# Optimization experiments

Measured on AMD Instinct MI355X. Metric: run time of the kernel, lower is better.

Reference implementation:

```python
import jax, jax.numpy as jnp
import numpy as np

NUM_HEADS = 8
HEAD_DIM = 64
AVG_K_LENGTH = 20
SCALE = 1.0 / (HEAD_DIM ** 0.5 * float(np.log(AVG_K_LENGTH)))  # 1/(sqrt(dim)*log(avg_k_length))


def setup_inputs() -> dict:
    key = jax.random.key(0)
    k1, k2, k3, k4 = jax.random.split(key, 4)
    B, HD, LQ, LK = 4, NUM_HEADS * HEAD_DIM, 2048, 2048
    q = jax.random.normal(k1, (B, HD, LQ), dtype=jnp.float32)
    k = jax.random.normal(k2, (B, HD, LK), dtype=jnp.float32)
    v = jax.random.normal(k3, (B, HD, LK), dtype=jnp.float32)
    k_length = jax.random.randint(k4, (B,), 512, LK + 1, dtype=jnp.int32)
    return {"q": q, "k": k, "v": v, "k_length": k_length}


def reference(q, k, v, k_length):
    b, hd, lq = q.shape
    lk = k.shape[-1]
    d = hd // NUM_HEADS
    # b (h d) l -> b h d l
    qh = q.reshape(b, NUM_HEADS, d, lq)
    kh = k.reshape(b, NUM_HEADS, d, lk)
    vh = v.reshape(b, NUM_HEADS, d, lk)
    # per-batch entropy-invariance scale: scale * log(k_length)
    s = SCALE * jnp.log(k_length.astype(jnp.float32))[:, None, None, None]  # (b,1,1,1)
    attn = jnp.einsum('bhdq,bhdk->bhqk', qh, kh)  # (b,h,lq,lk)
    attn = jax.nn.softmax(s * attn, axis=-1)
    out = jnp.einsum('bhqk,bhdk->bhdq', attn, vh)  # (b,h,d,lq)
    return out.reshape(b, hd, lq)
```

## Files before the change

kernel.cpp:

```cpp
#include <hip/hip_runtime.h>
#include <hip/hip_bf16.h>
#include <math.h>


typedef __attribute__((ext_vector_type(8))) short short8_t;
typedef __attribute__((ext_vector_type(4))) short short4_t;
typedef __attribute__((ext_vector_type(4))) float float4_t;
typedef __attribute__((ext_vector_type(16))) float float16_t;

#define SEQ   2048
#define NBH   32
#define NKT   32

__device__ __forceinline__ unsigned f2bf2u(float a, float b) {
#if __has_builtin(__builtin_amdgcn_cvt_pk_bf16_f32)
  typedef __bf16 bf16x2_t __attribute__((ext_vector_type(2)));
  union { bf16x2_t v; unsigned u; } cv;
  cv.v = __builtin_amdgcn_cvt_pk_bf16_f32(a, b);
  return cv.u;
#else
  union { float f; unsigned u; } x, y;
  x.f = a; y.f = b;
  unsigned ra = x.u + 0x7fffu + ((x.u >> 16) & 1u);
  unsigned rb = y.u + 0x7fffu + ((y.u >> 16) & 1u);
  return (ra >> 16) | (rb & 0xffff0000u);
#endif
}

__device__ __forceinline__ short f2bf1(float a) {
  return (short)(f2bf2u(a, a) & 0xffffu);
}

__device__ __forceinline__ float fast_exp2(float x) {
#if __has_builtin(__builtin_amdgcn_exp2f)
  return __builtin_amdgcn_exp2f(x);
#else
  return exp2f(x);
#endif
}

__device__ __forceinline__ void gld16(const void* g, void* l) {
  __builtin_amdgcn_global_load_lds(
      (const __attribute__((address_space(1))) void*)g,
      (__attribute__((address_space(3))) void*)l, 16, 0, 0);
}

__device__ __forceinline__ float4_t mfma32(short8_t a, short8_t b, float4_t c) {
  return __builtin_amdgcn_mfma_f32_16x16x32_bf16(a, b, c, 0, 0, 0);
}

__device__ __forceinline__ float16_t mfma3232(short8_t a, short8_t b, float16_t c) {
  return __builtin_amdgcn_mfma_f32_32x32x16_bf16(a, b, c, 0, 0, 0);
}

__device__ __forceinline__ void plswap(unsigned& a, unsigned& b, int hi) {
#if __has_builtin(__builtin_amdgcn_permlane32_swap)
  typedef __attribute__((ext_vector_type(2))) unsigned uint2_t;
  uint2_t r = __builtin_amdgcn_permlane32_swap(a, b, false, false);
  a = r[0]; b = r[1];
#else
  const unsigned sa = (unsigned)__shfl_xor((int)a, 32);
  const unsigned sb = (unsigned)__shfl_xor((int)b, 32);
  const unsigned an = hi ? sb : a;
  const unsigned bn = hi ? b : sa;
  a = an; b = bn;
#endif
}

#define PST 68
__global__ __launch_bounds__(256, 8)
void eia_prep_kernel(const float* __restrict__ kg, const float* __restrict__ vg,
                     unsigned short* __restrict__ Kt2, unsigned short* __restrict__ Vt2) {
  __shared__ __align__(16) short T[64 * PST];
  const int bh = blockIdx.x >> 5;
  const int kt = blockIdx.x & 31;
  const int t  = threadIdx.x;

  {
    const int dr = t >> 4;
    const int kq = (t & 15) * 4;
#pragma unroll
    for (int i = 0; i < 4; ++i) {
      const int d = i * 16 + dr;
      const float4_t f = *(const float4_t*)
          &kg[((size_t)bh * 64 + d) * SEQ + (size_t)(kt * 64 + kq)];
      T[(kq + 0) * PST + d] = f2bf1(f[0]);
      T[(kq + 1) * PST + d] = f2bf1(f[1]);
      T[(kq + 2) * PST + d] = f2bf1(f[2]);
      T[(kq + 3) * PST + d] = f2bf1(f[3]);
    }
  }
  __syncthreads();
  {
    unsigned short* outt = Kt2 + (size_t)(bh * 32 + kt) * 4096;
#pragma unroll
    for (int rep = 0; rep < 2; ++rep) {
      const int id2 = rep * 256 + t;
      const int lr = id2 & 63, ch = id2 >> 6;
      union { short8_t v; short4_t h[2]; } o;
      o.h[0] = *(const short4_t*)&T[lr * PST + ch * 8];
      o.h[1] = *(const short4_t*)&T[lr * PST + ch * 8 + 4];
      *(short8_t*)&outt[ch * 512 + lr * 8] = o.v;
    }
  }
  __syncthreads();

#pragma unroll
  for (int rep = 0; rep < 4; ++rep) {
    const int id2 = rep * 256 + t;
    const int d = id2 >> 4, l4 = (id2 & 15) * 4;
    const float4_t f = *(const float4_t*)
        &vg[((size_t)bh * 64 + d) * SEQ + (size_t)(kt * 64 + l4)];
    union { short4_t s; unsigned u[2]; } p;
    p.u[0] = f2bf2u(f[0], f[1]);
    p.u[1] = f2bf2u(f[2], f[3]);
    *(short4_t*)&T[d * PST + l4] = p.s;
  }
  __syncthreads();
  {
    unsigned short* outt = Vt2 + (size_t)(bh * 32 + kt) * 4096;
#pragma unroll
    for (int rep = 0; rep < 2; ++rep) {
      const int c = rep * 256 + t;
      const int kc = c >> 6, d = c & 63;
      union { short8_t v; short4_t h[2]; } o;
      o.h[0] = *(const short4_t*)&T[d * PST + kc * 8];
      o.h[1] = *(const short4_t*)&T[d * PST + kc * 8 + 4];
      *(short8_t*)&outt[c * 8] = o.v;
    }
  }
}

__global__ __launch_bounds__(256, 2)
void eia_attn_kernel(const float* __restrict__ qg,
                     const unsigned short* __restrict__ Kt2,
                     const unsigned short* __restrict__ Vt2,
                     const int* __restrict__ klen,
                     float* __restrict__ outg) {
  __shared__ __align__(16) short SM[24576];

  const int tid   = threadIdx.x;
  const int bh    = blockIdx.x & 31;
  const int qt    = blockIdx.x >> 5;
  const int q0    = qt * 128;
  const int qw    = tid >> 6;
  const int lane  = tid & 63;
  const int l31   = lane & 31;
  const int hi    = lane >> 5;

  const float c = (1.4426950408889634f / (8.0f * 2.9957322735539909f)) *
                  logf((float)klen[bh >> 3]);
  const size_t qb = (size_t)bh * 64 * SEQ;

#pragma unroll
  for (int rep = 0; rep < 8; ++rep) {
    const int id = rep * 256 + tid;
    const int d  = id >> 5;
    const int q4 = (id & 31) * 4;
    const float4_t f = *(const float4_t*)&qg[qb + (size_t)d * SEQ + (size_t)(q0 + q4)];
    SM[(q4 + 0) * 68 + d] = f2bf1(c * f[0]);
    SM[(q4 + 1) * 68 + d] = f2bf1(c * f[1]);
    SM[(q4 + 2) * 68 + d] = f2bf1(c * f[2]);
    SM[(q4 + 3) * 68 + d] = f2bf1(c * f[3]);
  }
  __syncthreads();

  short8_t qfrag[4];
#pragma unroll
  for (int s = 0; s < 4; ++s) {
    const short* qp = &SM[(qw * 32 + l31) * 68 + s * 16 + hi * 8];
    const short4_t lo = *(const short4_t*)qp;
    const short4_t hh = *(const short4_t*)(qp + 4);
    qfrag[s] = short8_t{lo[0], lo[1], lo[2], lo[3], hh[0], hh[1], hh[2], hh[3]};
  }
  __syncthreads();

  const char* ksrc = (const char*)Kt2 + (size_t)bh * NKT * 8192 + (2 * qw) * 1024 + lane * 16;
  const char* vsrc = (const char*)Vt2 + (size_t)bh * NKT * 8192 + (2 * qw) * 1024 + lane * 16;
  short* const kdst = &SM[(2 * qw) * 512];
  short* const vdst = &SM[12288 + (2 * qw) * 512];

  const int lofs = hi * 512 + l31 * 8;

  const float16_t z16 = {0.f,0.f,0.f,0.f,0.f,0.f,0.f,0.f,
                         0.f,0.f,0.f,0.f,0.f,0.f,0.f,0.f};
  float16_t oacc0 = z16, oacc1 = z16;
  float ls = 0.f;

  gld16(ksrc, kdst);               gld16(ksrc + 1024, kdst + 512);
  gld16(vsrc, vdst);               gld16(vsrc + 1024, vdst + 512);
  gld16(ksrc + 8192, kdst + 4096); gld16(ksrc + 8192 + 1024, kdst + 4096 + 512);
  gld16(vsrc + 8192, vdst + 4096); gld16(vsrc + 8192 + 1024, vdst + 4096 + 512);
  asm volatile("s_waitcnt vmcnt(0)" ::: "memory");

  int  sc = 0;
  int  sn = 2;
  size_t gsrc = 2 * 8192;

  for (int kt = 0; kt < NKT; ++kt) {
    if (kt < NKT - 1) asm volatile("s_waitcnt vmcnt(4)" ::: "memory");
    else              asm volatile("s_waitcnt vmcnt(0)" ::: "memory");
    asm volatile("s_barrier" ::: "memory");

    if (kt < NKT - 2) {
      const int so = sn * 4096;
      gld16(ksrc + gsrc, kdst + so); gld16(ksrc + gsrc + 1024, kdst + so + 512);
      gld16(vsrc + gsrc, vdst + so); gld16(vsrc + gsrc + 1024, vdst + so + 512);
      gsrc += 8192;
      sn = (sn == 2) ? 0 : sn + 1;
    }
    const int koff = sc * 4096;
    sc = (sc == 2) ? 0 : sc + 1;
    const short* const kb_ = &SM[koff + lofs];
    const short* const vb_ = &SM[12288 + koff + lofs];

    float16_t s0 = z16, s1 = z16;
#pragma unroll
    for (int s = 0; s < 4; ++s)
      s0 = mfma3232(*(const short8_t*)(kb_ + s * 1024), qfrag[s], s0);
#pragma unroll
    for (int s = 0; s < 4; ++s)
      s1 = mfma3232(*(const short8_t*)(kb_ + 256 + s * 1024), qfrag[s], s1);

    union pfu { short8_t s8; unsigned u[4]; };
    pfu pf[4];
#pragma unroll
    for (int kb = 0; kb < 2; ++kb) {
      float e[16];
#pragma unroll
      for (int r = 0; r < 16; ++r)
        e[r] = fast_exp2(kb == 0 ? s0[r] : s1[r]);
      ls += (((e[0] + e[1]) + (e[2] + e[3])) + ((e[4] + e[5]) + (e[6] + e[7]))) +
            (((e[8] + e[9]) + (e[10] + e[11])) + ((e[12] + e[13]) + (e[14] + e[15])));
#pragma unroll
      for (int ksl = 0; ksl < 2; ++ksl) {
        const int b = ksl * 8;
        unsigned a02 = f2bf2u(e[b + 0], e[b + 1]);
        unsigned b02 = f2bf2u(e[b + 4], e[b + 5]);
        unsigned a13 = f2bf2u(e[b + 2], e[b + 3]);
        unsigned b13 = f2bf2u(e[b + 6], e[b + 7]);
        plswap(a02, b02, hi);
        plswap(a13, b13, hi);
        pf[kb * 2 + ksl].u[0] = a02;
        pf[kb * 2 + ksl].u[1] = a13;
        pf[kb * 2 + ksl].u[2] = b02;
        pf[kb * 2 + ksl].u[3] = b13;
      }
    }

#pragma unroll
    for (int ks = 0; ks < 4; ++ks)
      oacc0 = mfma3232(*(const short8_t*)(vb_ + ks * 1024), pf[ks].s8, oacc0);
#pragma unroll
    for (int ks = 0; ks < 4; ++ks)
      oacc1 = mfma3232(*(const short8_t*)(vb_ + 256 + ks * 1024), pf[ks].s8, oacc1);
  }

  const float lst = ls + __shfl_xor(ls, 32);
  const float inv = 1.0f / lst;
  const size_t ob = qb + (size_t)(q0 + qw * 32 + l31);
#pragma unroll
  for (int r = 0; r < 16; ++r) {
    const int drow = (r & 3) + 8 * (r >> 2) + 4 * hi;
    outg[ob + (size_t)(drow) * SEQ]      = oacc0[r] * inv;
    outg[ob + (size_t)(drow + 32) * SEQ] = oacc1[r] * inv;
  }
}

#define DPAD  72
#define PPAD  68
__global__ __launch_bounds__(256, 5)
void eia_attn_fb(const float* __restrict__ qg, const float* __restrict__ kg,
                 const float* __restrict__ vg, const int* __restrict__ klen,
                 float* __restrict__ outg) {
  __shared__ __align__(16) short QPs[64 * DPAD];
  __shared__ __align__(16) short Ksf[64 * DPAD];
  __shared__ __align__(16) short Vsf[64 * DPAD];

  const int tid  = threadIdx.x;
  const int bh   = blockIdx.x & 31;
  const int qt   = blockIdx.x >> 5;
  const int q0   = qt * 64;
  const int w    = tid >> 6;
  const int lane = tid & 63;
  const int quad = lane >> 4;
  const int l16  = lane & 15;

  const size_t base = (size_t)bh * 64 * SEQ;
  const float c = (1.4426950408889634f / (8.0f * 2.9957322735539909f)) *
                  logf((float)klen[bh >> 3]);

#pragma unroll
  for (int it = 0; it < 2; ++it) {
    const int e = it * 4 + w;
    float f[8];
#pragma unroll
    for (int j = 0; j < 8; ++j)
      f[j] = c * qg[base + (size_t)(e * 8 + j) * SEQ + (size_t)(q0 + lane)];
    union { short8_t s8; unsigned u[4]; } t;
#pragma unroll
    for (int j = 0; j < 4; ++j) t.u[j] = f2bf2u(f[2 * j], f[2 * j + 1]);
    *(short8_t*)&QPs[lane * DPAD + e * 8] = t.s8;
  }
  __syncthreads();

  short8_t qfrag[2];
#pragma unroll
  for (int s = 0; s < 2; ++s)
    qfrag[s] = *(const short8_t*)&QPs[(w * 16 + l16) * DPAD + s * 32 + quad * 8];

  float4_t oacc[4];
#pragma unroll
  for (int t = 0; t < 4; ++t) { oacc[t][0] = 0.f; oacc[t][1] = 0.f; oacc[t][2] = 0.f; oacc[t][3] = 0.f; }
  float lsumv[4] = {0.f, 0.f, 0.f, 0.f};
  const int pbase = w * (16 * DPAD);

  for (int kt = 0; kt < NKT; ++kt) {
    const int k0 = kt * 64;
#pragma unroll
    for (int it = 0; it < 2; ++it) {
      float f[8];
#pragma unroll
      for (int j = 0; j < 8; ++j)
        f[j] = kg[base + (size_t)((it * 4 + w) * 8 + j) * SEQ + (size_t)(k0 + lane)];
      union { short8_t s8; unsigned u[4]; } t;
#pragma unroll
      for (int j = 0; j < 4; ++j) t.u[j] = f2bf2u(f[2 * j], f[2 * j + 1]);
      *(short8_t*)&Ksf[lane * DPAD + (it * 4 + w) * 8] = t.s8;
    }
#pragma unroll
    for (int it = 0; it < 4; ++it) {
      const int d = it * 16 + (w << 2) + (lane >> 4);
      const float4_t vv = *(const float4_t*)&vg[base + (size_t)d * SEQ + (size_t)(k0 + ((lane & 15) << 2))];
      union { short4_t s4; unsigned u[2]; } t;
      t.u[0] = f2bf2u(vv[0], vv[1]);
      t.u[1] = f2bf2u(vv[2], vv[3]);
      *(short4_t*)&Vsf[d * DPAD + ((lane & 15) << 2)] = t.s4;
    }
    __syncthreads();

    float4_t sacc[4];
#pragma unroll
    for (int t = 0; t < 4; ++t) { sacc[t][0] = 0.f; sacc[t][1] = 0.f; sacc[t][2] = 0.f; sacc[t][3] = 0.f; }
#pragma unroll
    for (int t = 0; t < 4; ++t)
#pragma unroll
      for (int s = 0; s < 2; ++s) {
        const short8_t bf = *(const short8_t*)&Ksf[(t * 16 + l16) * DPAD + s * 32 + quad * 8];
        sacc[t] = mfma32(qfrag[s], bf, sacc[t]);
      }

#pragma unroll
    for (int r = 0; r < 4; ++r) {
      const float p0 = fast_exp2(sacc[0][r]);
      const float p1 = fast_exp2(sacc[1][r]);
      const float p2 = fast_exp2(sacc[2][r]);
      const float p3 = fast_exp2(sacc[3][r]);
      lsumv[r] += (p0 + p1) + (p2 + p3);
      const int prow = pbase + (quad * 4 + r) * PPAD + l16;
      QPs[prow +  0] = f2bf1(p0);
      QPs[prow + 16] = f2bf1(p1);
      QPs[prow + 32] = f2bf1(p2);
      QPs[prow + 48] = f2bf1(p3);
    }

#pragma unroll
    for (int s = 0; s < 2; ++s) {
      const short* pr = &QPs[pbase + l16 * PPAD + s * 32 + quad * 8];
      const short4_t plo = *(const short4_t*)pr;
      const short4_t phi = *(const short4_t*)(pr + 4);
      const short8_t pfv = {plo[0], plo[1], plo[2], plo[3], phi[0], phi[1], phi[2], phi[3]};
#pragma unroll
      for (int t = 0; t < 4; ++t) {
        const short8_t vf = *(const short8_t*)&Vsf[(t * 16 + l16) * DPAD + s * 32 + quad * 8];
        oacc[t] = mfma32(pfv, vf, oacc[t]);
      }
    }
    __syncthreads();
  }

  float inv[4];
#pragma unroll
  for (int r = 0; r < 4; ++r) {
    float v = lsumv[r];
    v += __shfl_xor(v, 1);
    v += __shfl_xor(v, 2);
    v += __shfl_xor(v, 4);
    v += __shfl_xor(v, 8);
    inv[r] = 1.0f / v;
  }
#pragma unroll
  for (int t = 0; t < 4; ++t)
#pragma unroll
    for (int r = 0; r < 4; ++r)
      outg[base + (size_t)(t * 16 + l16) * SEQ +
           (size_t)(q0 + w * 16 + quad * 4 + r)] = oacc[t][r] * inv[r];
}

extern "C" void kernel_launch(void* const* d_in, const int* in_sizes, int n_in,
                              void* d_out, int out_size, void* d_ws, size_t ws_size,
                              hipStream_t stream) {
  const float* q  = (const float*)d_in[0];
  const float* k  = (const float*)d_in[1];
  const float* v  = (const float*)d_in[2];
  const int*   kl = (const int*)d_in[3];
  float* out = (float*)d_out;

  const size_t TEN  = (size_t)NBH * SEQ * 64;
  const size_t need = 2 * TEN * sizeof(unsigned short);

  if (ws_size >= need) {
    unsigned short* Kt2 = (unsigned short*)d_ws;
    unsigned short* Vt2 = Kt2 + TEN;
    eia_prep_kernel<<<1024, 256, 0, stream>>>(k, v, Kt2, Vt2);
    eia_attn_kernel<<<512, 256, 0, stream>>>(q, Kt2, Vt2, kl, out);
  } else {
    eia_attn_fb<<<1024, 256, 0, stream>>>(q, k, v, kl, out);
  }
}
```

Baseline: 139.6 us.

## Halve attention block size and load V directly into registers with double buffering

Each block now has 2 waves covering 64 queries, down from 4 waves covering 128, and twice as many blocks are launched. V tiles no longer pass through LDS: each lane loads its V fragments from global memory into registers, double-buffered one tile ahead, while K still goes through a 3-stage LDS ring. The aim is to free LDS and raise occupancy, and to drop the LDS traffic for V. In exchange each wave loads its own copy of V, which duplicates global/L2 traffic, raises register pressure, and makes every iteration wait with vmcnt(0) on the full V prefetch.

```diff
diff --git a/kernel.cpp b/kernel.cpp
--- a/kernel.cpp
+++ b/kernel.cpp
@@ -131,18 +131,18 @@
   }
 }
 
-__global__ __launch_bounds__(256, 2)
+__global__ __launch_bounds__(128, 2)
 void eia_attn_kernel(const float* __restrict__ qg,
                      const unsigned short* __restrict__ Kt2,
                      const unsigned short* __restrict__ Vt2,
                      const int* __restrict__ klen,
                      float* __restrict__ outg) {
-  __shared__ __align__(16) short SM[24576];
+  __shared__ __align__(16) short SM[12288];
 
   const int tid   = threadIdx.x;
   const int bh    = blockIdx.x & 31;
   const int qt    = blockIdx.x >> 5;
-  const int q0    = qt * 128;
+  const int q0    = qt * 64;
   const int qw    = tid >> 6;
   const int lane  = tid & 63;
   const int l31   = lane & 31;
@@ -154,9 +154,9 @@
 
 #pragma unroll
   for (int rep = 0; rep < 8; ++rep) {
-    const int id = rep * 256 + tid;
-    const int d  = id >> 5;
-    const int q4 = (id & 31) * 4;
+    const int id = rep * 128 + tid;
+    const int d  = id >> 4;
+    const int q4 = (id & 15) * 4;
     const float4_t f = *(const float4_t*)&qg[qb + (size_t)d * SEQ + (size_t)(q0 + q4)];
     SM[(q4 + 0) * 68 + d] = f2bf1(c * f[0]);
     SM[(q4 + 1) * 68 + d] = f2bf1(c * f[1]);
@@ -175,86 +175,109 @@
   }
   __syncthreads();
 
-  const char* ksrc = (const char*)Kt2 + (size_t)bh * NKT * 8192 + (2 * qw) * 1024 + lane * 16;
-  const char* vsrc = (const char*)Vt2 + (size_t)bh * NKT * 8192 + (2 * qw) * 1024 + lane * 16;
-  short* const kdst = &SM[(2 * qw) * 512];
-  short* const vdst = &SM[12288 + (2 * qw) * 512];
+  const char* ksrc = (const char*)Kt2 + (size_t)bh * NKT * 8192 + (4 * qw) * 1024 + lane * 16;
+  short* const kdst = &SM[(4 * qw) * 512];
 
   const int lofs = hi * 512 + l31 * 8;
+  const short* const kfp = &SM[lofs];
+
+  const char* const vgl = (const char*)Vt2 + (size_t)bh * NKT * 8192 +
+                          hi * 1024 + l31 * 16;
 
   const float16_t z16 = {0.f,0.f,0.f,0.f,0.f,0.f,0.f,0.f,
                          0.f,0.f,0.f,0.f,0.f,0.f,0.f,0.f};
   float16_t oacc0 = z16, oacc1 = z16;
   float ls = 0.f;
 
-  gld16(ksrc, kdst);               gld16(ksrc + 1024, kdst + 512);
-  gld16(vsrc, vdst);               gld16(vsrc + 1024, vdst + 512);
-  gld16(ksrc + 8192, kdst + 4096); gld16(ksrc + 8192 + 1024, kdst + 4096 + 512);
-  gld16(vsrc + 8192, vdst + 4096); gld16(vsrc + 8192 + 1024, vdst + 4096 + 512);
-  asm volatile("s_waitcnt vmcnt(0)" ::: "memory");
+  short8_t vA[8], vB[8];
+
+#pragma unroll
+  for (int i = 0; i < 4; ++i) gld16(ksrc + i * 1024, kdst + i * 512);
+#pragma unroll
+  for (int i = 0; i < 4; ++i) gld16(ksrc + 8192 + i * 1024, kdst + 4096 + i * 512);
+#pragma unroll
+  for (int dt = 0; dt < 2; ++dt)
+#pragma unroll
+    for (int ks = 0; ks < 4; ++ks)
+      vA[dt * 4 + ks] = *(const short8_t*)(vgl + dt * 512 + ks * 2048);
 
   int  sc = 0;
   int  sn = 2;
   size_t gsrc = 2 * 8192;
 
-  for (int kt = 0; kt < NKT; ++kt) {
-    if (kt < NKT - 1) asm volatile("s_waitcnt vmcnt(4)" ::: "memory");
-    else              asm volatile("s_waitcnt vmcnt(0)" ::: "memory");
-    asm volatile("s_barrier" ::: "memory");
-
-    if (kt < NKT - 2) {
-      const int so = sn * 4096;
-      gld16(ksrc + gsrc, kdst + so); gld16(ksrc + gsrc + 1024, kdst + so + 512);
-      gld16(vsrc + gsrc, vdst + so); gld16(vsrc + gsrc + 1024, vdst + so + 512);
-      gsrc += 8192;
-      sn = (sn == 2) ? 0 : sn + 1;
-    }
-    const int koff = sc * 4096;
-    sc = (sc == 2) ? 0 : sc + 1;
-    const short* const kb_ = &SM[koff + lofs];
-    const short* const vb_ = &SM[12288 + koff + lofs];
-
-    float16_t s0 = z16, s1 = z16;
-#pragma unroll
-    for (int s = 0; s < 4; ++s)
-      s0 = mfma3232(*(const short8_t*)(kb_ + s * 1024), qfrag[s], s0);
-#pragma unroll
-    for (int s = 0; s < 4; ++s)
-      s1 = mfma3232(*(const short8_t*)(kb_ + 256 + s * 1024), qfrag[s], s1);
-
-    union pfu { short8_t s8; unsigned u[4]; };
-    pfu pf[4];
-#pragma unroll
-    for (int kb = 0; kb < 2; ++kb) {
-      float e[16];
-#pragma unroll
-      for (int r = 0; r < 16; ++r)
-        e[r] = fast_exp2(kb == 0 ? s0[r] : s1[r]);
-      ls += (((e[0] + e[1]) + (e[2] + e[3])) + ((e[4] + e[5]) + (e[6] + e[7]))) +
-            (((e[8] + e[9]) + (e[10] + e[11])) + ((e[12] + e[13]) + (e[14] + e[15])));
-#pragma unroll
-      for (int ksl = 0; ksl < 2; ++ksl) {
-        const int b = ksl * 8;
-        unsigned a02 = f2bf2u(e[b + 0], e[b + 1]);
-        unsigned b02 = f2bf2u(e[b + 4], e[b + 5]);
-        unsigned a13 = f2bf2u(e[b + 2], e[b + 3]);
-        unsigned b13 = f2bf2u(e[b + 6], e[b + 7]);
-        plswap(a02, b02, hi);
-        plswap(a13, b13, hi);
-        pf[kb * 2 + ksl].u[0] = a02;
-        pf[kb * 2 + ksl].u[1] = a13;
-        pf[kb * 2 + ksl].u[2] = b02;
-        pf[kb * 2 + ksl].u[3] = b13;
-      }
-    }
-
-#pragma unroll
-    for (int ks = 0; ks < 4; ++ks)
-      oacc0 = mfma3232(*(const short8_t*)(vb_ + ks * 1024), pf[ks].s8, oacc0);
-#pragma unroll
-    for (int ks = 0; ks < 4; ++ks)
-      oacc1 = mfma3232(*(const short8_t*)(vb_ + 256 + ks * 1024), pf[ks].s8, oacc1);
-  }
+#define EIA_BODY(KT, VC, VN)                                                  \
+  do {                                                                        \
+    asm volatile("s_waitcnt vmcnt(0)" ::: "memory");                          \
+    asm volatile("s_barrier" ::: "memory");                                   \
+    if ((KT) < NKT - 2) {                                                     \
+      const int so = sn * 4096;                                               \
+      _Pragma("unroll")                                                       \
+      for (int i = 0; i < 4; ++i)                                             \
+        gld16(ksrc + gsrc + i * 1024, kdst + so + i * 512);                   \
+      gsrc += 8192;                                                           \
+      sn = (sn == 2) ? 0 : sn + 1;                                            \
+    }                                                                         \
+    if ((KT) < NKT - 1) {                                                     \
+      const char* vp = vgl + (size_t)((KT) + 1) * 8192;                       \
+      _Pragma("unroll")                                                       \
+      for (int dt = 0; dt < 2; ++dt)                                          \
+        _Pragma("unroll")                                                     \
+        for (int ks = 0; ks < 4; ++ks)                                        \
+          VN[dt * 4 + ks] = *(const short8_t*)(vp + dt * 512 + ks * 2048);    \
+    }                                                                         \
+    const int koff = sc * 4096;                                               \
+    sc = (sc == 2) ? 0 : sc + 1;                                              \
+    const short* const kb_ = kfp + koff;                                      \
+                   \
+    float16_t s0 = z16, s1 = z16;                                             \
+    _Pragma("unroll")                                                         \
+    for (int s = 0; s < 4; ++s)                                               \
+      s0 = mfma3232(*(const short8_t*)(kb_ + s * 1024), qfrag[s], s0);        \
+    _Pragma("unroll")                                                         \
+    for (int s = 0; s < 4; ++s)                                               \
+      s1 = mfma3232(*(const short8_t*)(kb_ + 256 + s * 1024), qfrag[s], s1);  \
+               \
+    union pfu { short8_t s8; unsigned u[4]; };                                \
+    pfu pf[4];                                                                \
+    _Pragma("unroll")                                                         \
+    for (int kb = 0; kb < 2; ++kb) {                                          \
+      float e[16];                                                            \
+      _Pragma("unroll")                                                       \
+      for (int r = 0; r < 16; ++r)                                            \
+        e[r] = fast_exp2(kb == 0 ? s0[r] : s1[r]);                            \
+      ls += (((e[0] + e[1]) + (e[2] + e[3])) +                                \
+             ((e[4] + e[5]) + (e[6] + e[7]))) +                               \
+            (((e[8] + e[9]) + (e[10] + e[11])) +                              \
+             ((e[12] + e[13]) + (e[14] + e[15])));                            \
+      _Pragma("unroll")                                                       \
+      for (int ksl = 0; ksl < 2; ++ksl) {                                     \
+        const int b = ksl * 8;                                                \
+        unsigned a02 = f2bf2u(e[b + 0], e[b + 1]);                            \
+        unsigned b02 = f2bf2u(e[b + 4], e[b + 5]);                            \
+        unsigned a13 = f2bf2u(e[b + 2], e[b + 3]);                            \
+        unsigned b13 = f2bf2u(e[b + 6], e[b + 7]);                            \
+        plswap(a02, b02, hi);                                                 \
+        plswap(a13, b13, hi);                                                 \
+        pf[kb * 2 + ksl].u[0] = a02;                                          \
+        pf[kb * 2 + ksl].u[1] = a13;                                          \
+        pf[kb * 2 + ksl].u[2] = b02;                                          \
+        pf[kb * 2 + ksl].u[3] = b13;                                          \
+      }                                                                       \
+    }                                                                         \
+           \
+    _Pragma("unroll")                                                         \
+    for (int ks = 0; ks < 4; ++ks)                                            \
+      oacc0 = mfma3232(VC[ks], pf[ks].s8, oacc0);                             \
+    _Pragma("unroll")                                                         \
+    for (int ks = 0; ks < 4; ++ks)                                            \
+      oacc1 = mfma3232(VC[4 + ks], pf[ks].s8, oacc1);                         \
+  } while (0)
+
+  for (int kt = 0; kt < NKT; kt += 2) {
+    EIA_BODY(kt,     vA, vB);
+    EIA_BODY(kt + 1, vB, vA);
+  }
+#undef EIA_BODY
 
   const float lst = ls + __shfl_xor(ls, 32);
   const float inv = 1.0f / lst;
@@ -413,7 +436,7 @@
     unsigned short* Kt2 = (unsigned short*)d_ws;
     unsigned short* Vt2 = Kt2 + TEN;
     eia_prep_kernel<<<1024, 256, 0, stream>>>(k, v, Kt2, Vt2);
-    eia_attn_kernel<<<512, 256, 0, stream>>>(q, Kt2, Vt2, kl, out);
+    eia_attn_kernel<<<1024, 128, 0, stream>>>(q, Kt2, Vt2, kl, out);
   } else {
     eia_attn_fb<<<1024, 256, 0, stream>>>(q, k, v, kl, out);
   }
```

Measured after the change: 145.8 us. 4.4% more time.

## Split each key tile across two wave halves and reduce partial outputs in LDS

Applied to the files above, without the earlier changes.

Doubles the attention block from 256 to 512 threads. Each query wave pair splits the 64-key tile into two 32-key halves, so each wave does half the QK MFMAs, exps and PV MFMAs per iteration. Each thread now issues only one K and one V global-to-LDS load per tile. At the end the second half writes its partial accumulators and row sums to shared memory, and the first half adds them and stores the output. This raises the number of waves available to hide latency, at the cost of an extra reduction, more barriers and higher occupancy demands.

```diff
diff --git a/kernel.cpp b/kernel.cpp
--- a/kernel.cpp
+++ b/kernel.cpp
@@ -131,7 +131,7 @@
   }
 }
 
-__global__ __launch_bounds__(256, 2)
+__global__ __launch_bounds__(512, 4)
 void eia_attn_kernel(const float* __restrict__ qg,
                      const unsigned short* __restrict__ Kt2,
                      const unsigned short* __restrict__ Vt2,
@@ -143,7 +143,9 @@
   const int bh    = blockIdx.x & 31;
   const int qt    = blockIdx.x >> 5;
   const int q0    = qt * 128;
-  const int qw    = tid >> 6;
+  const int wv    = tid >> 6;
+  const int qw    = wv & 3;
+  const int h     = wv >> 2;
   const int lane  = tid & 63;
   const int l31   = lane & 31;
   const int hi    = lane >> 5;
@@ -153,8 +155,8 @@
   const size_t qb = (size_t)bh * 64 * SEQ;
 
 #pragma unroll
-  for (int rep = 0; rep < 8; ++rep) {
-    const int id = rep * 256 + tid;
+  for (int rep = 0; rep < 4; ++rep) {
+    const int id = rep * 512 + tid;
     const int d  = id >> 5;
     const int q4 = (id & 31) * 4;
     const float4_t f = *(const float4_t*)&qg[qb + (size_t)d * SEQ + (size_t)(q0 + q4)];
@@ -175,22 +177,22 @@
   }
   __syncthreads();
 
-  const char* ksrc = (const char*)Kt2 + (size_t)bh * NKT * 8192 + (2 * qw) * 1024 + lane * 16;
-  const char* vsrc = (const char*)Vt2 + (size_t)bh * NKT * 8192 + (2 * qw) * 1024 + lane * 16;
-  short* const kdst = &SM[(2 * qw) * 512];
-  short* const vdst = &SM[12288 + (2 * qw) * 512];
+  const char* ksrc = (const char*)Kt2 + (size_t)bh * NKT * 8192 + wv * 1024 + lane * 16;
+  const char* vsrc = (const char*)Vt2 + (size_t)bh * NKT * 8192 + wv * 1024 + lane * 16;
+  short* const kdst = &SM[wv * 512];
+  short* const vdst = &SM[12288 + wv * 512];
 
   const int lofs = hi * 512 + l31 * 8;
+  const short* const kfp = &SM[lofs + h * 256];
+  const short* const vfp = &SM[12288 + lofs];
 
   const float16_t z16 = {0.f,0.f,0.f,0.f,0.f,0.f,0.f,0.f,
                          0.f,0.f,0.f,0.f,0.f,0.f,0.f,0.f};
   float16_t oacc0 = z16, oacc1 = z16;
   float ls = 0.f;
 
-  gld16(ksrc, kdst);               gld16(ksrc + 1024, kdst + 512);
-  gld16(vsrc, vdst);               gld16(vsrc + 1024, vdst + 512);
-  gld16(ksrc + 8192, kdst + 4096); gld16(ksrc + 8192 + 1024, kdst + 4096 + 512);
-  gld16(vsrc + 8192, vdst + 4096); gld16(vsrc + 8192 + 1024, vdst + 4096 + 512);
+  gld16(ksrc, kdst);               gld16(vsrc, vdst);
+  gld16(ksrc + 8192, kdst + 4096); gld16(vsrc + 8192, vdst + 4096);
   asm volatile("s_waitcnt vmcnt(0)" ::: "memory");
 
   int  sc = 0;
@@ -198,72 +200,93 @@
   size_t gsrc = 2 * 8192;
 
   for (int kt = 0; kt < NKT; ++kt) {
-    if (kt < NKT - 1) asm volatile("s_waitcnt vmcnt(4)" ::: "memory");
+    if (kt < NKT - 1) asm volatile("s_waitcnt vmcnt(2)" ::: "memory");
     else              asm volatile("s_waitcnt vmcnt(0)" ::: "memory");
     asm volatile("s_barrier" ::: "memory");
 
     if (kt < NKT - 2) {
       const int so = sn * 4096;
-      gld16(ksrc + gsrc, kdst + so); gld16(ksrc + gsrc + 1024, kdst + so + 512);
-      gld16(vsrc + gsrc, vdst + so); gld16(vsrc + gsrc + 1024, vdst + so + 512);
+      gld16(ksrc + gsrc, kdst + so);
+      gld16(vsrc + gsrc, vdst + so);
       gsrc += 8192;
       sn = (sn == 2) ? 0 : sn + 1;
     }
     const int koff = sc * 4096;
     sc = (sc == 2) ? 0 : sc + 1;
-    const short* const kb_ = &SM[koff + lofs];
-    const short* const vb_ = &SM[12288 + koff + lofs];
-
-    float16_t s0 = z16, s1 = z16;
+    const short* const kb_ = kfp + koff;
+    const short* const vb_ = vfp + koff;
+
+    float16_t s0 = z16;
 #pragma unroll
     for (int s = 0; s < 4; ++s)
       s0 = mfma3232(*(const short8_t*)(kb_ + s * 1024), qfrag[s], s0);
-#pragma unroll
-    for (int s = 0; s < 4; ++s)
-      s1 = mfma3232(*(const short8_t*)(kb_ + 256 + s * 1024), qfrag[s], s1);
-
+
+    float e[16];
+#pragma unroll
+    for (int r = 0; r < 16; ++r) e[r] = fast_exp2(s0[r]);
+    ls += (((e[0] + e[1]) + (e[2] + e[3])) + ((e[4] + e[5]) + (e[6] + e[7]))) +
+          (((e[8] + e[9]) + (e[10] + e[11])) + ((e[12] + e[13]) + (e[14] + e[15])));
     union pfu { short8_t s8; unsigned u[4]; };
-    pfu pf[4];
-#pragma unroll
-    for (int kb = 0; kb < 2; ++kb) {
-      float e[16];
-#pragma unroll
-      for (int r = 0; r < 16; ++r)
-        e[r] = fast_exp2(kb == 0 ? s0[r] : s1[r]);
-      ls += (((e[0] + e[1]) + (e[2] + e[3])) + ((e[4] + e[5]) + (e[6] + e[7]))) +
-            (((e[8] + e[9]) + (e[10] + e[11])) + ((e[12] + e[13]) + (e[14] + e[15])));
-#pragma unroll
-      for (int ksl = 0; ksl < 2; ++ksl) {
-        const int b = ksl * 8;
-        unsigned a02 = f2bf2u(e[b + 0], e[b + 1]);
-        unsigned b02 = f2bf2u(e[b + 4], e[b + 5]);
-        unsigned a13 = f2bf2u(e[b + 2], e[b + 3]);
-        unsigned b13 = f2bf2u(e[b + 6], e[b + 7]);
-        plswap(a02, b02, hi);
-        plswap(a13, b13, hi);
-        pf[kb * 2 + ksl].u[0] = a02;
-        pf[kb * 2 + ksl].u[1] = a13;
-        pf[kb * 2 + ksl].u[2] = b02;
-        pf[kb * 2 + ksl].u[3] = b13;
-      }
-    }
-
-#pragma unroll
-    for (int ks = 0; ks < 4; ++ks)
-      oacc0 = mfma3232(*(const short8_t*)(vb_ + ks * 1024), pf[ks].s8, oacc0);
-#pragma unroll
-    for (int ks = 0; ks < 4; ++ks)
-      oacc1 = mfma3232(*(const short8_t*)(vb_ + 256 + ks * 1024), pf[ks].s8, oacc1);
-  }
-
-  const float lst = ls + __shfl_xor(ls, 32);
-  const float inv = 1.0f / lst;
-  const size_t ob = qb + (size_t)(q0 + qw * 32 + l31);
-#pragma unroll
-  for (int r = 0; r < 16; ++r) {
-    const int drow = (r & 3) + 8 * (r >> 2) + 4 * hi;
-    outg[ob + (size_t)(drow) * SEQ]      = oacc0[r] * inv;
-    outg[ob + (size_t)(drow + 32) * SEQ] = oacc1[r] * inv;
+    pfu pf[2];
+#pragma unroll
+    for (int ksl = 0; ksl < 2; ++ksl) {
+      const int b = ksl * 8;
+      unsigned a02 = f2bf2u(e[b + 0], e[b + 1]);
+      unsigned b02 = f2bf2u(e[b + 4], e[b + 5]);
+      unsigned a13 = f2bf2u(e[b + 2], e[b + 3]);
+      unsigned b13 = f2bf2u(e[b + 6], e[b + 7]);
+      plswap(a02, b02, hi);
+      plswap(a13, b13, hi);
+      pf[ksl].u[0] = a02;
+      pf[ksl].u[1] = a13;
+      pf[ksl].u[2] = b02;
+      pf[ksl].u[3] = b13;
+    }
+
+#pragma unroll
+    for (int ksl = 0; ksl < 2; ++ksl)
+      oacc0 = mfma3232(*(const short8_t*)(vb_ + (h * 2 + ksl) * 1024),
+                       pf[ksl].s8, oacc0);
+#pragma unroll
+    for (int ksl = 0; ksl < 2; ++ksl)
+      oacc1 = mfma3232(*(const short8_t*)(vb_ + 256 + (h * 2 + ksl) * 1024),
+                       pf[ksl].s8, oacc1);
+  }
+
+  __syncthreads();
+  union o16 { float16_t v; float4_t q[4]; };
+  float* const FA = (float*)SM;
+  float* const fb = FA + (size_t)(qw * 64 + lane) * 34;
+  if (h == 1) {
+    o16 a; a.v = oacc0;
+    o16 b2; b2.v = oacc1;
+#pragma unroll
+    for (int i = 0; i < 4; ++i) *(float4_t*)(fb + i * 4)      = a.q[i];
+#pragma unroll
+    for (int i = 0; i < 4; ++i) *(float4_t*)(fb + 16 + i * 4) = b2.q[i];
+    fb[32] = ls;
+  }
+  __syncthreads();
+  if (h == 0) {
+    o16 a; a.v = oacc0;
+    o16 b2; b2.v = oacc1;
+#pragma unroll
+    for (int i = 0; i < 4; ++i) {
+      const float4_t p0 = *(const float4_t*)(fb + i * 4);
+      const float4_t p1 = *(const float4_t*)(fb + 16 + i * 4);
+      a.q[i][0] += p0[0]; a.q[i][1] += p0[1]; a.q[i][2] += p0[2]; a.q[i][3] += p0[3];
+      b2.q[i][0] += p1[0]; b2.q[i][1] += p1[1]; b2.q[i][2] += p1[2]; b2.q[i][3] += p1[3];
+    }
+    const float lsc = ls + fb[32];
+    const float lst = lsc + __shfl_xor(lsc, 32);
+    const float inv = 1.0f / lst;
+    const size_t ob = qb + (size_t)(q0 + qw * 32 + l31);
+#pragma unroll
+    for (int r = 0; r < 16; ++r) {
+      const int drow = (r & 3) + 8 * (r >> 2) + 4 * hi;
+      outg[ob + (size_t)(drow) * SEQ]      = a.v[r] * inv;
+      outg[ob + (size_t)(drow + 32) * SEQ] = b2.v[r] * inv;
+    }
   }
 }
 
@@ -413,7 +436,7 @@
     unsigned short* Kt2 = (unsigned short*)d_ws;
     unsigned short* Vt2 = Kt2 + TEN;
     eia_prep_kernel<<<1024, 256, 0, stream>>>(k, v, Kt2, Vt2);
-    eia_attn_kernel<<<512, 256, 0, stream>>>(q, Kt2, Vt2, kl, out);
+    eia_attn_kernel<<<512, 512, 0, stream>>>(q, Kt2, Vt2, kl, out);
   } else {
     eia_attn_fb<<<1024, 256, 0, stream>>>(q, k, v, kl, out);
   }
```

Result: no change. 137.8 us (-1.3%).
